# Kernel optimization log

Measured on AMD Instinct MI355X. Metric: run time of the kernel, lower is better.

Reference implementation:

```python
import jax, jax.numpy as jnp
import numpy as np

CODEBOOK_SIZE = 8192
LATENT_DIM = 256
COMMIT_W = 0.25
B, H, W = 32, 32, 32


def setup_inputs() -> dict:
    key = jax.random.key(0)
    kz, ke = jax.random.split(key)
    z = jax.random.normal(kz, (B, LATENT_DIM, H, W), dtype=jnp.float32)
    # torch init: uniform(-1/K, 1/K)
    emb = jax.random.uniform(ke, (CODEBOOK_SIZE, LATENT_DIM), dtype=jnp.float32,
                             minval=-1.0 / CODEBOOK_SIZE, maxval=1.0 / CODEBOOK_SIZE)
    return {"z": z, "emb": emb}


def reference(z, emb):
    # (B,C,H,W) -> (B,H,W,C)
    zp = jnp.transpose(z, (0, 2, 3, 1))
    zf = zp.reshape(-1, LATENT_DIM)                      # (N, D)
    # squared-distance via expansion: ||z||^2 + ||e||^2 - 2 z.e
    d = (jnp.sum(zf * zf, axis=1, keepdims=True)
         + jnp.sum(emb * emb, axis=1)[None, :]
         - 2.0 * jnp.matmul(zf, emb.T))                  # (N, K)
    idx = jnp.argmin(d, axis=1)                          # (N,)
    z_q = emb[idx].reshape(zp.shape)                     # (B,H,W,C)
    zq_sg = jax.lax.stop_gradient(z_q)
    z_sg = jax.lax.stop_gradient(zp)
    codebook_loss = (COMMIT_W * jnp.mean((zq_sg - zp) ** 2)
                     + jnp.mean((z_q - z_sg) ** 2))
    # straight-through estimator
    z_q_st = zp + jax.lax.stop_gradient(z_q - zp)
    quantized = jnp.transpose(z_q_st, (0, 3, 1, 2))      # (B,C,H,W)
    indices = idx.reshape(zp.shape[:-1])                 # (B,H,W)
    return quantized, indices, codebook_loss
```

## Files before the change

### kernel.cpp

```cpp
#include <hip/hip_runtime.h>

typedef _Float16 half_t;
typedef _Float16 half8 __attribute__((ext_vector_type(8)));
typedef _Float16 half2_t __attribute__((ext_vector_type(2)));
typedef float f32x4 __attribute__((ext_vector_type(4)));
typedef unsigned long long ull;

#define K_CODES 8192
#define D_DIM   256
#define N_PTS   32768
#define HW      1024
#define CHW     262144
#define B_      32
#define W_      32

#define OFF_IDX  8388608
#define OFF_LOSS 8421376

#define KSPLIT 4
#define KRANGE 2048
#define NCHUNK 32
#define W_WIN  1.5e-4f
#define WX_SEL 0.63f
#define CAP_BKT 2048

#define WS_E16  0x000000u
#define WS_E2   0x400000u
#define WS_Z2   0x408000u
#define WS_FLAG 0x428000u
#define WS_SEL8 0x450000u
#define WS_SCNT 0x490000u
#define WS_PART 0x4B0000u
#define WS_BCNT 0x4B2000u
#define DO_CMAX  0x000000u
#define DO_ENT   0x000000u
#define DO_PTOP  0x100000u
#define DO_CAND  0x500000u
#define DO_FSCAN 0x900000u
#define DO_CCNT  0x920000u
#define DO_Z16   0x1000000u

__device__ __forceinline__ unsigned int mono_enc(float f) {
    unsigned int u = __float_as_uint(f);
    return (u & 0x80000000u) ? ~u : (u | 0x80000000u);
}
__device__ __forceinline__ float mono_dec(unsigned int m) {
    unsigned int u = (m & 0x80000000u) ? (m ^ 0x80000000u) : ~m;
    return __uint_as_float(u);
}
__device__ __forceinline__ void glds16(const void* g, void* l) {
    __builtin_amdgcn_global_load_lds(
        (const __attribute__((address_space(1))) unsigned int*)g,
        (__attribute__((address_space(3))) unsigned int*)l, 16, 0, 0);
}

union u32h2 { unsigned int u; half2_t h; };
__device__ __forceinline__ half2_t h2(unsigned int u) { u32h2 t; t.u = u; return t.h; }

#if __has_builtin(__builtin_amdgcn_fdot2)
__device__ __forceinline__ float fdot2_(half2_t a, half2_t b, float c) {
    return __builtin_amdgcn_fdot2(a, b, c, false);
}
#else
__device__ __forceinline__ float fdot2_(half2_t a, half2_t b, float c) {
    return fmaf((float)a.x, (float)b.x, fmaf((float)a.y, (float)b.y, c));
}
#endif

__device__ __forceinline__ float red8np(const float* r) {
    return __fadd_rn(__fadd_rn(__fadd_rn(r[0], r[1]), __fadd_rn(r[2], r[3])),
                     __fadd_rn(__fadd_rn(r[4], r[5]), __fadd_rn(r[6], r[7])));
}

__global__ __launch_bounds__(256) void convert_kernel(
        const float* __restrict__ emb, char* __restrict__ e16, float* __restrict__ e2,
        const float* __restrict__ z, half_t* __restrict__ z16, float* __restrict__ z2,
        int* __restrict__ flags) {
    const int bx = blockIdx.x;
    if (bx < 32) {
        if (bx == 0 && threadIdx.x == 0) flags[0] = 0;
        const int k = bx * 256 + threadIdx.x;
        const float4* row = (const float4*)(emb + (size_t)k * D_DIM);
        char* dst = e16 + (size_t)(k >> 6) * 32768 + (size_t)(k & 63) * 16;
        float r[8], h1 = 0.f;
        #pragma unroll 4
        for (int s = 0; s < 32; s++) {
            if (s == 16) { h1 = red8np(r); }
            const float4 v0 = row[s * 2];
            const float4 v1 = row[s * 2 + 1];
            union { half_t h[8]; uint4 u; } t;
            t.h[0] = (half_t)(v0.x * 8192.0f); t.h[1] = (half_t)(v0.y * 8192.0f);
            t.h[2] = (half_t)(v0.z * 8192.0f); t.h[3] = (half_t)(v0.w * 8192.0f);
            t.h[4] = (half_t)(v1.x * 8192.0f); t.h[5] = (half_t)(v1.y * 8192.0f);
            t.h[6] = (half_t)(v1.z * 8192.0f); t.h[7] = (half_t)(v1.w * 8192.0f);
            *(uint4*)(dst + (size_t)s * 1024) = t.u;
            const float q0 = __fmul_rn(v0.x, v0.x), q1 = __fmul_rn(v0.y, v0.y);
            const float q2 = __fmul_rn(v0.z, v0.z), q3 = __fmul_rn(v0.w, v0.w);
            const float q4 = __fmul_rn(v1.x, v1.x), q5 = __fmul_rn(v1.y, v1.y);
            const float q6 = __fmul_rn(v1.z, v1.z), q7 = __fmul_rn(v1.w, v1.w);
            if (s == 0 || s == 16) {
                r[0] = q0; r[1] = q1; r[2] = q2; r[3] = q3;
                r[4] = q4; r[5] = q5; r[6] = q6; r[7] = q7;
            } else {
                r[0] = __fadd_rn(r[0], q0); r[1] = __fadd_rn(r[1], q1);
                r[2] = __fadd_rn(r[2], q2); r[3] = __fadd_rn(r[3], q3);
                r[4] = __fadd_rn(r[4], q4); r[5] = __fadd_rn(r[5], q5);
                r[6] = __fadd_rn(r[6], q6); r[7] = __fadd_rn(r[7], q7);
            }
        }
        e2[k] = __fadd_rn(h1, red8np(r));
    } else {
        const int pt = (bx - 32) * 256 + threadIdx.x;
        const float* zp = z + (size_t)(pt >> 10) * CHW + (pt & (HW - 1));
        half_t* dst = z16 + (size_t)pt * 256;
        float hs[2];
        #pragma unroll
        for (int hb = 0; hb < 2; hb++) {
            float r[8];
            #pragma unroll
            for (int d0 = 0; d0 < 128; d0 += 8) {
                union { half_t h[8]; uint4 u; } t;
                #pragma unroll
                for (int j = 0; j < 8; j++) {
                    const float v = zp[(size_t)(hb * 128 + d0 + j) * HW];
                    t.h[j] = (half_t)v;
                    const float sq = __fmul_rn(v, v);
                    r[j] = (d0 == 0) ? sq : __fadd_rn(r[j], sq);
                }
                *(uint4*)(dst + hb * 128 + d0) = t.u;
            }
            hs[hb] = red8np(r);
        }
        z2[pt] = __fadd_rn(hs[0], hs[1]);
    }
}

__global__ __launch_bounds__(512, 4) void pass1_kernel(
        const half_t* __restrict__ z16, const uint4* __restrict__ e16,
        float* __restrict__ cmax) {
    __shared__ __align__(16) char sA[65536];
    const int tid  = threadIdx.x;
    const int lane = tid & 63;
    const int wave = tid >> 6;
    const int col  = lane & 15;
    const int quad = lane >> 4;
    const int bx = blockIdx.x, by = blockIdx.y;
    const int p0 = bx * 256;
    const int kbase = by * KRANGE;

    half8 zb[2][8];
    #pragma unroll
    for (int n = 0; n < 2; n++) {
        const int pt = p0 + wave * 32 + n * 16 + col;
        const char* src = (const char*)z16 + (size_t)pt * 512 + quad * 16;
        #pragma unroll
        for (int ks = 0; ks < 8; ks++)
            zb[n][ks] = *(const half8*)(src + ks * 64);
    }

    const char* esrc = (const char*)e16 + (size_t)kbase * 512;
    {
        const char* s0 = esrc + wave * 4096 + lane * 16;
        char* d0 = sA + wave * 4096;
        #pragma unroll
        for (int i = 0; i < 4; i++) glds16(s0 + i * 1024, d0 + i * 1024);
    }
    __syncthreads();

    int cur = 0;
    for (int c = 0; c < NCHUNK; ++c) {
        if (c + 1 < NCHUNK) {
            const char* s0 = esrc + (size_t)(c + 1) * 32768 + wave * 4096 + lane * 16;
            char* d0 = sA + (cur ^ 1) * 32768 + wave * 4096;
            #pragma unroll
            for (int i = 0; i < 4; i++) glds16(s0 + i * 1024, d0 + i * 1024);
        }
        f32x4 acc[4][2];
        #pragma unroll
        for (int m = 0; m < 4; m++)
            #pragma unroll
            for (int n = 0; n < 2; n++) acc[m][n] = (f32x4){0.f, 0.f, 0.f, 0.f};

        const char* base = sA + cur * 32768 + col * 16;
        #pragma unroll
        for (int ks = 0; ks < 8; ks++) {
            const int so = (ks * 4 + quad) * 1024;
            half8 a[4];
            #pragma unroll
            for (int m = 0; m < 4; m++) a[m] = *(const half8*)(base + so + m * 256);
            #pragma unroll
            for (int m = 0; m < 4; m++)
                #pragma unroll
                for (int n = 0; n < 2; n++)
                    acc[m][n] = __builtin_amdgcn_mfma_f32_16x16x32_f16(a[m], zb[n][ks], acc[m][n], 0, 0, 0);
        }
        const int sub = by * NCHUNK + c;
        #pragma unroll
        for (int n = 0; n < 2; n++) {
            float xm = acc[0][n][0];
            #pragma unroll
            for (int m = 0; m < 4; m++)
                #pragma unroll
                for (int r = 0; r < 4; r++) xm = fmaxf(xm, acc[m][n][r]);
            xm = fmaxf(xm, __shfl_xor(xm, 16, 64));
            xm = fmaxf(xm, __shfl_xor(xm, 32, 64));
            if (quad == 0)
                cmax[(size_t)sub * N_PTS + p0 + wave * 32 + n * 16 + col] = xm;
        }
        __syncthreads();
        cur ^= 1;
    }
}

__global__ __launch_bounds__(256) void stageb_kernel(
        const float* __restrict__ cmax, ull* __restrict__ sel8, int* __restrict__ scnt,
        unsigned* __restrict__ bcnt) {
    if (threadIdx.x == 0) bcnt[blockIdx.x] = 0u;
    if (blockIdx.x == 0 && threadIdx.x == 1) bcnt[128] = 0u;
    const int pt = blockIdx.x * 256 + threadIdx.x;
    float xmax = -3.0e38f;
    #pragma unroll 8
    for (int s = 0; s < 128; s++) xmax = fmaxf(xmax, cmax[(size_t)s * N_PTS + pt]);
    const float cut = xmax - WX_SEL;
    ull pack = 0; int cnt = 0;
    for (int s = 0; s < 128; s++) {
        if (cmax[(size_t)s * N_PTS + pt] >= cut) {
            if (cnt < 8) pack |= ((ull)(unsigned)s) << (8 * cnt);
            cnt++;
        }
    }
    sel8[pt] = pack; scnt[pt] = cnt;
}

__global__ __launch_bounds__(256) void stageb2_kernel(
        const ull* __restrict__ sel8, int* __restrict__ scnt,
        unsigned* __restrict__ bcnt, unsigned* __restrict__ ent,
        unsigned* __restrict__ fslist, unsigned* __restrict__ ccnt) {
    const int pt = blockIdx.x * 256 + threadIdx.x;
    ccnt[pt] = 0u;
    const int cnt = scnt[pt];
    bool ok = (cnt >= 1 && cnt <= 8);
    if (ok) {
        const ull s8 = sel8[pt];
        for (int j = 0; j < cnt; j++) {
            const int s = (int)((s8 >> (8 * j)) & 0xFFu);
            const unsigned pos = atomicAdd(&bcnt[s], 1u);
            if (pos >= CAP_BKT) { ok = false; break; }
            ent[s * CAP_BKT + pos] = (unsigned)pt | ((unsigned)j << 16);
        }
    }
    if (!ok) {
        const unsigned mp = atomicAdd(&bcnt[128], 1u);
        fslist[mp] = (unsigned)pt;
        scnt[pt] = -1;
    }
}

__global__ __launch_bounds__(256) void stagec3_kernel(
        const half_t* __restrict__ z16, const uint4* __restrict__ e16,
        const unsigned* __restrict__ bcnt, const unsigned* __restrict__ ent,
        ull* __restrict__ ptop, unsigned* __restrict__ cand,
        unsigned* __restrict__ ccnt) {
    __shared__ __align__(16) unsigned int zslot[4][128];
    const int tid = threadIdx.x, lane = tid & 63, wave = tid >> 6;
    const int c = blockIdx.x & 127, part = blockIdx.x >> 7;
    const int npart = gridDim.x >> 7;
    const unsigned cnt = min(bcnt[c], (unsigned)CAP_BKT);
    if (cnt == 0) return;
    const int code = c * 64 + lane;
    uint4 e[32];
    {
        const uint4* er = e16 + (size_t)(code >> 6) * 2048 + (code & 63);
        #pragma unroll
        for (int j = 0; j < 32; j++) e[j] = er[(size_t)j * 64];
    }
    const char* zb = (const char*)&zslot[wave][0];
    for (unsigned i = (unsigned)(part * 4 + wave); i < cnt; i += (unsigned)(npart * 4)) {
        const unsigned ev = ent[c * CAP_BKT + i];
        const int pt = (int)(ev & 0xFFFFu);
        const int j  = (int)((ev >> 16) & 7u);
        {
            const uint2 w = *(const uint2*)((const char*)z16 + (size_t)pt * 512 + lane * 8);
            *(uint2*)((char*)&zslot[wave][0] + lane * 8) = w;
        }
        __threadfence_block();
        float x0 = 0.f, x1 = 0.f, x2 = 0.f, x3 = 0.f, x4 = 0.f, x5 = 0.f, x6 = 0.f, x7 = 0.f;
        #pragma unroll
        for (int q = 0; q < 32; q += 2) {
            const uint4 z0 = *(const uint4*)(zb + q * 16);
            const uint4 z1 = *(const uint4*)(zb + q * 16 + 16);
            x0 = fdot2_(h2(e[q].x),     h2(z0.x), x0);
            x1 = fdot2_(h2(e[q].y),     h2(z0.y), x1);
            x2 = fdot2_(h2(e[q].z),     h2(z0.z), x2);
            x3 = fdot2_(h2(e[q].w),     h2(z0.w), x3);
            x4 = fdot2_(h2(e[q + 1].x), h2(z1.x), x4);
            x5 = fdot2_(h2(e[q + 1].y), h2(z1.y), x5);
            x6 = fdot2_(h2(e[q + 1].z), h2(z1.z), x6);
            x7 = fdot2_(h2(e[q + 1].w), h2(z1.w), x7);
        }
        const float sc = (((x0 + x1) + (x2 + x3)) + ((x4 + x5) + (x6 + x7))) * (-2.0f / 8192.0f);
        ull r1 = ((ull)mono_enc(sc) << 32) | (unsigned)code;
        ull r2 = ~0ull;
        #pragma unroll
        for (int s = 1; s < 64; s <<= 1) {
            const ull o1 = __shfl_xor(r1, s, 64);
            const ull o2 = __shfl_xor(r2, s, 64);
            if (o1 < r1) { r2 = (r1 < o2) ? r1 : o2; r1 = o1; }
            else         { r2 = (o1 < r2) ? o1 : r2; }
        }
        if (lane == 0) {
            ptop[(size_t)(pt * 8 + j) * 2 + 0] = r1;
            ptop[(size_t)(pt * 8 + j) * 2 + 1] = r2;
        }
        const float v1 = mono_dec((unsigned)(r1 >> 32));
        const bool in = sc < v1 + W_WIN;
        const ull m = __ballot(in);
        int base = 0;
        if (lane == 0) base = (int)atomicAdd(&ccnt[pt], (unsigned)__popcll(m));
        base = __shfl(base, 0, 64);
        const int p = base + (int)__popcll(m & ((1ull << lane) - 1ull));
        if (in && p < 32) cand[(size_t)pt * 32 + p] = (unsigned)code;
    }
}

__global__ __launch_bounds__(256) void mergec_kernel(
        const ull* __restrict__ ptop, const int* __restrict__ scnt,
        int* __restrict__ flags, float* __restrict__ dout) {
    const int pt = blockIdx.x * 256 + threadIdx.x;
    const int cnt = scnt[pt];
    if (cnt < 1 || cnt > 8) return;
    ull b1 = ~0ull, b2 = ~0ull;
    for (int j = 0; j < cnt; j++) {
        #pragma unroll
        for (int t = 0; t < 2; t++) {
            const ull v = ptop[(size_t)(pt * 8 + j) * 2 + t];
            if (v < b1) { b2 = b1; b1 = v; } else if (v < b2) b2 = v;
        }
    }
    dout[OFF_IDX + pt] = (float)(unsigned)(b1 & 0xFFFFFFFFu);
    const float v1 = mono_dec((unsigned)(b1 >> 32));
    const float v2 = mono_dec((unsigned)(b2 >> 32));
    if (v2 - v1 < W_WIN) {
        const int pos = atomicAdd(flags, 1);
        flags[16 + pos] = pt;
    }
}

__global__ __launch_bounds__(256) void refine_kernel(
        const float* __restrict__ z, const float* __restrict__ emb,
        const float* __restrict__ e2, const float* __restrict__ z2,
        const unsigned* __restrict__ cand, const unsigned* __restrict__ candcnt,
        const int* __restrict__ flags, const unsigned* __restrict__ fslist,
        const unsigned* __restrict__ bcnt, float* __restrict__ dout) {
    __shared__ float zl[4][256];
    const int tid = threadIdx.x, lane = tid & 63, wave = tid >> 6;
    const int gw = blockIdx.x * 4 + wave;
    const int nw = gridDim.x * 4;
    const int count = flags[0];
    for (int f = gw; f < count; f += nw) {
        const int n = flags[16 + f];
        const float* zp = z + (size_t)(n >> 10) * CHW + (n & (HW - 1));
        #pragma unroll
        for (int q = 0; q < 4; q++)
            zl[wave][lane + 64 * q] = zp[(size_t)(lane + 64 * q) * HW];
        __threadfence_block();
        int cc = (int)candcnt[n]; if (cc > 32) cc = 32;
        float d; int k;
        if (lane < cc) {
            k = (int)cand[(size_t)n * 32 + lane];
            const float* ep = emb + (size_t)k * D_DIM;
            float m = 0.f;
            for (int c = 0; c < D_DIM; c++) m = fmaf(zl[wave][c], ep[c], m);
            d = __fsub_rn(__fadd_rn(z2[n], e2[k]), __fmul_rn(2.0f, m));
        } else { d = 3.0e38f; k = 1 << 20; }
        #pragma unroll
        for (int s = 1; s < 32; s <<= 1) {
            const float od = __shfl_xor(d, s, 64);
            const int   ok = __shfl_xor(k, s, 64);
            if (od < d || (od == d && ok < k)) { d = od; k = ok; }
        }
        if (lane == 0) dout[OFF_IDX + n] = (float)k;
    }
    const int fscount = (int)bcnt[128];
    for (int f = gw; f < fscount; f += nw) {
        const int n = (int)fslist[f];
        const float* zp = z + (size_t)(n >> 10) * CHW + (n & (HW - 1));
        #pragma unroll
        for (int q = 0; q < 4; q++)
            zl[wave][lane + 64 * q] = zp[(size_t)(lane + 64 * q) * HW];
        __threadfence_block();
        float bd = 3.0e38f; int bk = 1 << 20;
        for (int t = 0; t < K_CODES / 64; t++) {
            const int k = t * 64 + lane;
            const float* ep = emb + (size_t)k * D_DIM;
            float m = 0.f;
            for (int c = 0; c < D_DIM; c++) m = fmaf(zl[wave][c], ep[c], m);
            const float d = __fsub_rn(__fadd_rn(z2[n], e2[k]), __fmul_rn(2.0f, m));
            if (d < bd) { bd = d; bk = k; }
        }
        #pragma unroll
        for (int s = 1; s < 64; s <<= 1) {
            const float od = __shfl_xor(bd, s, 64);
            const int   ok = __shfl_xor(bk, s, 64);
            if (od < bd || (od == bd && ok < bk)) { bd = od; bk = ok; }
        }
        if (lane == 0) dout[OFF_IDX + n] = (float)bk;
    }
}

__global__ __launch_bounds__(256) void gather_kernel(
        const float* __restrict__ z, const float* __restrict__ emb,
        float* __restrict__ dout, float* __restrict__ partials) {
    __shared__ __align__(16) float qs[D_DIM][W_ + 1];
    __shared__ float red[4];
    const int bh = blockIdx.x;
    const int b = bh >> 5, h = bh & 31;
    const int tid = threadIdx.x;

    const float* idxf = dout + OFF_IDX + bh * W_;
    const int w  = tid >> 3;
    const int cq = tid & 7;
    const int idx_w = (int)idxf[w];
    const float* erow = emb + (size_t)idx_w * D_DIM;
    #pragma unroll
    for (int it = 0; it < 8; it++) {
        const int c4 = (it * 8 + cq) * 4;
        float4 v = *(const float4*)(erow + c4);
        qs[c4 + 0][w] = v.x; qs[c4 + 1][w] = v.y;
        qs[c4 + 2][w] = v.z; qs[c4 + 3][w] = v.w;
    }
    __syncthreads();

    const int w2 = tid & 31, cg = tid >> 5;
    float ss = 0.f;
    const float* zbh = z    + (size_t)b * CHW + h * W_;
    float*       obh = dout + (size_t)b * CHW + h * W_;
    #pragma unroll
    for (int it = 0; it < 32; it++) {
        const int c = cg * 32 + it;
        const float q  = qs[c][w2];
        const float zv = zbh[(size_t)c * HW + w2];
        obh[(size_t)c * HW + w2] = q;
        const float dd = q - zv;
        ss = fmaf(dd, dd, ss);
    }
    #pragma unroll
    for (int m = 1; m < 64; m <<= 1) ss += __shfl_xor(ss, m, 64);
    const int lane = tid & 63, wv = tid >> 6;
    if (lane == 0) red[wv] = ss;
    __syncthreads();
    if (tid == 0) partials[bh] = red[0] + red[1] + red[2] + red[3];
}

__global__ void loss_kernel(const float* __restrict__ partials, float* __restrict__ dout) {
    __shared__ float sv[256];
    const int tid = threadIdx.x;
    float s = 0.f;
    #pragma unroll
    for (int i = 0; i < 4; i++) s += partials[tid + 256 * i];
    sv[tid] = s;
    __syncthreads();
    for (int st = 128; st > 0; st >>= 1) {
        if (tid < st) sv[tid] += sv[tid + st];
        __syncthreads();
    }
    if (tid == 0) dout[OFF_LOSS] = sv[0] * (1.25f / 8388608.0f);
}

extern "C" void kernel_launch(void* const* d_in, const int* in_sizes, int n_in,
                              void* d_out, int out_size, void* d_ws, size_t ws_size,
                              hipStream_t stream) {
    const float* z   = (const float*)d_in[0];
    const float* emb = (const float*)d_in[1];
    float* dout = (float*)d_out;

    char* ws  = (char*)d_ws;
    char* dob = (char*)d_out;
    uint4*  e16   = (uint4*)(ws + WS_E16);
    float*  e2    = (float*)(ws + WS_E2);
    float*  z2    = (float*)(ws + WS_Z2);
    int*    flags = (int*)(ws + WS_FLAG);
    ull*    sel8  = (ull*)(ws + WS_SEL8);
    int*    scnt  = (int*)(ws + WS_SCNT);
    float*  part  = (float*)(ws + WS_PART);
    unsigned* bcnt = (unsigned*)(ws + WS_BCNT);
    float*    cmax  = (float*)(dob + DO_CMAX);
    half_t*   z16   = (half_t*)(dob + DO_Z16);
    unsigned* ent   = (unsigned*)(dob + DO_ENT);
    ull*      ptop  = (ull*)(dob + DO_PTOP);
    unsigned* cand  = (unsigned*)(dob + DO_CAND);
    unsigned* fslist= (unsigned*)(dob + DO_FSCAN);
    unsigned* ccnt  = (unsigned*)(dob + DO_CCNT);

    hipLaunchKernelGGL(convert_kernel, dim3(160),         dim3(256), 0, stream, emb, (char*)e16, e2, z, z16, z2, flags);
    hipLaunchKernelGGL(pass1_kernel,   dim3(128, KSPLIT), dim3(512), 0, stream, z16, e16, cmax);
    hipLaunchKernelGGL(stageb_kernel,  dim3(128),         dim3(256), 0, stream, cmax, sel8, scnt, bcnt);
    hipLaunchKernelGGL(stageb2_kernel, dim3(128),         dim3(256), 0, stream, sel8, scnt, bcnt, ent, fslist, ccnt);
    hipLaunchKernelGGL(stagec3_kernel, dim3(1024),        dim3(256), 0, stream, z16, e16, bcnt, ent, ptop, cand, ccnt);
    hipLaunchKernelGGL(mergec_kernel,  dim3(128),         dim3(256), 0, stream, ptop, scnt, flags, dout);
    hipLaunchKernelGGL(refine_kernel,  dim3(512),         dim3(256), 0, stream, z, emb, e2, z2, cand, ccnt, flags, fslist, bcnt, dout);
    hipLaunchKernelGGL(gather_kernel,  dim3(B_ * 32),     dim3(256), 0, stream, z, emb, dout, part);
    hipLaunchKernelGGL(loss_kernel,    dim3(1),           dim3(256), 0, stream, part, dout);
}
```

Baseline: 312.2 us.

## Fuse merge and refine kernels, atomic row max, and atomic loss reduction

Pass1 now keeps a per-point running max and publishes it with atomicMax into the index output area, so stageb no longer rescans all 128 cmax slices to find the max. The merge and refine kernels are combined into one wave-per-point kernel that either writes the winner directly, refines over the candidate list, or falls back to a full scan. The loss is accumulated with atomicAdd in gather, which removes the separate loss kernel. Two launches are dropped, but the fused kernel walks all 32768 points one wave at a time, which may load-balance worse than the flagged-list approach, and the float atomic loss sum is non-deterministic.

```diff
diff --git a/kernel.cpp b/kernel.cpp
--- a/kernel.cpp
+++ b/kernel.cpp
@@ -27,10 +27,8 @@
 #define WS_E16  0x000000u
 #define WS_E2   0x400000u
 #define WS_Z2   0x408000u
-#define WS_FLAG 0x428000u
 #define WS_SEL8 0x450000u
 #define WS_SCNT 0x490000u
-#define WS_PART 0x4B0000u
 #define WS_BCNT 0x4B2000u
 #define DO_CMAX  0x000000u
 #define DO_ENT   0x000000u
@@ -75,10 +73,10 @@
 __global__ __launch_bounds__(256) void convert_kernel(
         const float* __restrict__ emb, char* __restrict__ e16, float* __restrict__ e2,
         const float* __restrict__ z, half_t* __restrict__ z16, float* __restrict__ z2,
-        int* __restrict__ flags) {
+        float* __restrict__ dout) {
     const int bx = blockIdx.x;
     if (bx < 32) {
-        if (bx == 0 && threadIdx.x == 0) flags[0] = 0;
+        if (bx == 0 && threadIdx.x == 0) dout[OFF_LOSS] = 0.0f;
         const int k = bx * 256 + threadIdx.x;
         const float4* row = (const float4*)(emb + (size_t)k * D_DIM);
         char* dst = e16 + (size_t)(k >> 6) * 32768 + (size_t)(k & 63) * 16;
@@ -111,6 +109,7 @@
         e2[k] = __fadd_rn(h1, red8np(r));
     } else {
         const int pt = (bx - 32) * 256 + threadIdx.x;
+        ((unsigned*)(dout + OFF_IDX))[pt] = 0u;
         const float* zp = z + (size_t)(pt >> 10) * CHW + (pt & (HW - 1));
         half_t* dst = z16 + (size_t)pt * 256;
         float hs[2];
@@ -137,7 +136,7 @@
 
 __global__ __launch_bounds__(512, 4) void pass1_kernel(
         const half_t* __restrict__ z16, const uint4* __restrict__ e16,
-        float* __restrict__ cmax) {
+        float* __restrict__ cmax, unsigned* __restrict__ xatom) {
     __shared__ __align__(16) char sA[65536];
     const int tid  = threadIdx.x;
     const int lane = tid & 63;
@@ -167,6 +166,7 @@
     }
     __syncthreads();
 
+    float rmax[2] = {-3.0e38f, -3.0e38f};
     int cur = 0;
     for (int c = 0; c < NCHUNK; ++c) {
         if (c + 1 < NCHUNK) {
@@ -204,24 +204,27 @@
                 for (int r = 0; r < 4; r++) xm = fmaxf(xm, acc[m][n][r]);
             xm = fmaxf(xm, __shfl_xor(xm, 16, 64));
             xm = fmaxf(xm, __shfl_xor(xm, 32, 64));
+            rmax[n] = fmaxf(rmax[n], xm);
             if (quad == 0)
                 cmax[(size_t)sub * N_PTS + p0 + wave * 32 + n * 16 + col] = xm;
         }
         __syncthreads();
         cur ^= 1;
     }
+    if (quad == 0) {
+        #pragma unroll
+        for (int n = 0; n < 2; n++)
+            atomicMax(&xatom[p0 + wave * 32 + n * 16 + col], mono_enc(rmax[n]));
+    }
 }
 
 __global__ __launch_bounds__(256) void stageb_kernel(
-        const float* __restrict__ cmax, ull* __restrict__ sel8, int* __restrict__ scnt,
-        unsigned* __restrict__ bcnt) {
+        const float* __restrict__ cmax, const unsigned* __restrict__ xatom,
+        ull* __restrict__ sel8, int* __restrict__ scnt, unsigned* __restrict__ bcnt) {
     if (threadIdx.x == 0) bcnt[blockIdx.x] = 0u;
     if (blockIdx.x == 0 && threadIdx.x == 1) bcnt[128] = 0u;
     const int pt = blockIdx.x * 256 + threadIdx.x;
-    float xmax = -3.0e38f;
-    #pragma unroll 8
-    for (int s = 0; s < 128; s++) xmax = fmaxf(xmax, cmax[(size_t)s * N_PTS + pt]);
-    const float cut = xmax - WX_SEL;
+    const float cut = mono_dec(xatom[pt]) - WX_SEL;
     ull pack = 0; int cnt = 0;
     for (int s = 0; s < 128; s++) {
         if (cmax[(size_t)s * N_PTS + pt] >= cut) {
@@ -323,94 +326,83 @@
     }
 }
 
-__global__ __launch_bounds__(256) void mergec_kernel(
-        const ull* __restrict__ ptop, const int* __restrict__ scnt,
-        int* __restrict__ flags, float* __restrict__ dout) {
-    const int pt = blockIdx.x * 256 + threadIdx.x;
-    const int cnt = scnt[pt];
-    if (cnt < 1 || cnt > 8) return;
-    ull b1 = ~0ull, b2 = ~0ull;
-    for (int j = 0; j < cnt; j++) {
-        #pragma unroll
-        for (int t = 0; t < 2; t++) {
-            const ull v = ptop[(size_t)(pt * 8 + j) * 2 + t];
-            if (v < b1) { b2 = b1; b1 = v; } else if (v < b2) b2 = v;
-        }
-    }
-    dout[OFF_IDX + pt] = (float)(unsigned)(b1 & 0xFFFFFFFFu);
-    const float v1 = mono_dec((unsigned)(b1 >> 32));
-    const float v2 = mono_dec((unsigned)(b2 >> 32));
-    if (v2 - v1 < W_WIN) {
-        const int pos = atomicAdd(flags, 1);
-        flags[16 + pos] = pt;
-    }
-}
-
-__global__ __launch_bounds__(256) void refine_kernel(
+__global__ __launch_bounds__(256) void mergeref_kernel(
         const float* __restrict__ z, const float* __restrict__ emb,
         const float* __restrict__ e2, const float* __restrict__ z2,
-        const unsigned* __restrict__ cand, const unsigned* __restrict__ candcnt,
-        const int* __restrict__ flags, const unsigned* __restrict__ fslist,
-        const unsigned* __restrict__ bcnt, float* __restrict__ dout) {
+        const ull* __restrict__ ptop, const int* __restrict__ scnt,
+        const unsigned* __restrict__ cand, const unsigned* __restrict__ ccnt,
+        float* __restrict__ dout) {
     __shared__ float zl[4][256];
     const int tid = threadIdx.x, lane = tid & 63, wave = tid >> 6;
     const int gw = blockIdx.x * 4 + wave;
     const int nw = gridDim.x * 4;
-    const int count = flags[0];
-    for (int f = gw; f < count; f += nw) {
-        const int n = flags[16 + f];
-        const float* zp = z + (size_t)(n >> 10) * CHW + (n & (HW - 1));
-        #pragma unroll
-        for (int q = 0; q < 4; q++)
-            zl[wave][lane + 64 * q] = zp[(size_t)(lane + 64 * q) * HW];
-        __threadfence_block();
-        int cc = (int)candcnt[n]; if (cc > 32) cc = 32;
-        float d; int k;
-        if (lane < cc) {
-            k = (int)cand[(size_t)n * 32 + lane];
-            const float* ep = emb + (size_t)k * D_DIM;
-            float m = 0.f;
-            for (int c = 0; c < D_DIM; c++) m = fmaf(zl[wave][c], ep[c], m);
-            d = __fsub_rn(__fadd_rn(z2[n], e2[k]), __fmul_rn(2.0f, m));
-        } else { d = 3.0e38f; k = 1 << 20; }
-        #pragma unroll
-        for (int s = 1; s < 32; s <<= 1) {
-            const float od = __shfl_xor(d, s, 64);
-            const int   ok = __shfl_xor(k, s, 64);
-            if (od < d || (od == d && ok < k)) { d = od; k = ok; }
-        }
-        if (lane == 0) dout[OFF_IDX + n] = (float)k;
-    }
-    const int fscount = (int)bcnt[128];
-    for (int f = gw; f < fscount; f += nw) {
-        const int n = (int)fslist[f];
-        const float* zp = z + (size_t)(n >> 10) * CHW + (n & (HW - 1));
-        #pragma unroll
-        for (int q = 0; q < 4; q++)
-            zl[wave][lane + 64 * q] = zp[(size_t)(lane + 64 * q) * HW];
-        __threadfence_block();
-        float bd = 3.0e38f; int bk = 1 << 20;
-        for (int t = 0; t < K_CODES / 64; t++) {
-            const int k = t * 64 + lane;
-            const float* ep = emb + (size_t)k * D_DIM;
-            float m = 0.f;
-            for (int c = 0; c < D_DIM; c++) m = fmaf(zl[wave][c], ep[c], m);
-            const float d = __fsub_rn(__fadd_rn(z2[n], e2[k]), __fmul_rn(2.0f, m));
-            if (d < bd) { bd = d; bk = k; }
-        }
-        #pragma unroll
-        for (int s = 1; s < 64; s <<= 1) {
-            const float od = __shfl_xor(bd, s, 64);
-            const int   ok = __shfl_xor(bk, s, 64);
-            if (od < bd || (od == bd && ok < bk)) { bd = od; bk = ok; }
-        }
-        if (lane == 0) dout[OFF_IDX + n] = (float)bk;
+    for (int pt = gw; pt < N_PTS; pt += nw) {
+        const int cnt = scnt[pt];
+        if (cnt >= 1 && cnt <= 8) {
+            ull b1 = ~0ull, b2 = ~0ull;
+            for (int j = 0; j < cnt; j++) {
+                #pragma unroll
+                for (int t = 0; t < 2; t++) {
+                    const ull v = ptop[(size_t)(pt * 8 + j) * 2 + t];
+                    if (v < b1) { b2 = b1; b1 = v; } else if (v < b2) b2 = v;
+                }
+            }
+            const float v1 = mono_dec((unsigned)(b1 >> 32));
+            const float v2 = mono_dec((unsigned)(b2 >> 32));
+            if (v2 - v1 >= W_WIN) {
+                if (lane == 0) dout[OFF_IDX + pt] = (float)(unsigned)(b1 & 0xFFFFFFFFu);
+                continue;
+            }
+            const float* zp = z + (size_t)(pt >> 10) * CHW + (pt & (HW - 1));
+            #pragma unroll
+            for (int q = 0; q < 4; q++)
+                zl[wave][lane + 64 * q] = zp[(size_t)(lane + 64 * q) * HW];
+            __threadfence_block();
+            int cc = (int)ccnt[pt]; if (cc > 32) cc = 32;
+            float d; int k;
+            if (lane < cc) {
+                k = (int)cand[(size_t)pt * 32 + lane];
+                const float* ep = emb + (size_t)k * D_DIM;
+                float m = 0.f;
+                for (int c = 0; c < D_DIM; c++) m = fmaf(zl[wave][c], ep[c], m);
+                d = __fsub_rn(__fadd_rn(z2[pt], e2[k]), __fmul_rn(2.0f, m));
+            } else { d = 3.0e38f; k = 1 << 20; }
+            #pragma unroll
+            for (int s = 1; s < 32; s <<= 1) {
+                const float od = __shfl_xor(d, s, 64);
+                const int   ok = __shfl_xor(k, s, 64);
+                if (od < d || (od == d && ok < k)) { d = od; k = ok; }
+            }
+            if (lane == 0) dout[OFF_IDX + pt] = (float)k;
+        } else {
+            const float* zp = z + (size_t)(pt >> 10) * CHW + (pt & (HW - 1));
+            #pragma unroll
+            for (int q = 0; q < 4; q++)
+                zl[wave][lane + 64 * q] = zp[(size_t)(lane + 64 * q) * HW];
+            __threadfence_block();
+            float bd = 3.0e38f; int bk = 1 << 20;
+            for (int t = 0; t < K_CODES / 64; t++) {
+                const int k = t * 64 + lane;
+                const float* ep = emb + (size_t)k * D_DIM;
+                float m = 0.f;
+                for (int c = 0; c < D_DIM; c++) m = fmaf(zl[wave][c], ep[c], m);
+                const float d = __fsub_rn(__fadd_rn(z2[pt], e2[k]), __fmul_rn(2.0f, m));
+                if (d < bd) { bd = d; bk = k; }
+            }
+            #pragma unroll
+            for (int s = 1; s < 64; s <<= 1) {
+                const float od = __shfl_xor(bd, s, 64);
+                const int   ok = __shfl_xor(bk, s, 64);
+                if (od < bd || (od == bd && ok < bk)) { bd = od; bk = ok; }
+            }
+            if (lane == 0) dout[OFF_IDX + pt] = (float)bk;
+        }
     }
 }
 
 __global__ __launch_bounds__(256) void gather_kernel(
         const float* __restrict__ z, const float* __restrict__ emb,
-        float* __restrict__ dout, float* __restrict__ partials) {
+        float* __restrict__ dout) {
     __shared__ __align__(16) float qs[D_DIM][W_ + 1];
     __shared__ float red[4];
     const int bh = blockIdx.x;
@@ -449,22 +441,10 @@
     const int lane = tid & 63, wv = tid >> 6;
     if (lane == 0) red[wv] = ss;
     __syncthreads();
-    if (tid == 0) partials[bh] = red[0] + red[1] + red[2] + red[3];
-}
-
-__global__ void loss_kernel(const float* __restrict__ partials, float* __restrict__ dout) {
-    __shared__ float sv[256];
-    const int tid = threadIdx.x;
-    float s = 0.f;
-    #pragma unroll
-    for (int i = 0; i < 4; i++) s += partials[tid + 256 * i];
-    sv[tid] = s;
-    __syncthreads();
-    for (int st = 128; st > 0; st >>= 1) {
-        if (tid < st) sv[tid] += sv[tid + st];
-        __syncthreads();
-    }
-    if (tid == 0) dout[OFF_LOSS] = sv[0] * (1.25f / 8388608.0f);
+    if (tid == 0) {
+        const float t = red[0] + red[1] + red[2] + red[3];
+        atomicAdd(dout + OFF_LOSS, t * (1.25f / 8388608.0f));
+    }
 }
 
 extern "C" void kernel_launch(void* const* d_in, const int* in_sizes, int n_in,
@@ -479,10 +459,8 @@
     uint4*  e16   = (uint4*)(ws + WS_E16);
     float*  e2    = (float*)(ws + WS_E2);
     float*  z2    = (float*)(ws + WS_Z2);
-    int*    flags = (int*)(ws + WS_FLAG);
     ull*    sel8  = (ull*)(ws + WS_SEL8);
     int*    scnt  = (int*)(ws + WS_SCNT);
-    float*  part  = (float*)(ws + WS_PART);
     unsigned* bcnt = (unsigned*)(ws + WS_BCNT);
     float*    cmax  = (float*)(dob + DO_CMAX);
     half_t*   z16   = (half_t*)(dob + DO_Z16);
@@ -491,14 +469,13 @@
     unsigned* cand  = (unsigned*)(dob + DO_CAND);
     unsigned* fslist= (unsigned*)(dob + DO_FSCAN);
     unsigned* ccnt  = (unsigned*)(dob + DO_CCNT);
-
-    hipLaunchKernelGGL(convert_kernel, dim3(160),         dim3(256), 0, stream, emb, (char*)e16, e2, z, z16, z2, flags);
-    hipLaunchKernelGGL(pass1_kernel,   dim3(128, KSPLIT), dim3(512), 0, stream, z16, e16, cmax);
-    hipLaunchKernelGGL(stageb_kernel,  dim3(128),         dim3(256), 0, stream, cmax, sel8, scnt, bcnt);
+    unsigned* xatom = (unsigned*)(dout + OFF_IDX);
+
+    hipLaunchKernelGGL(convert_kernel, dim3(160),         dim3(256), 0, stream, emb, (char*)e16, e2, z, z16, z2, dout);
+    hipLaunchKernelGGL(pass1_kernel,   dim3(128, KSPLIT), dim3(512), 0, stream, z16, e16, cmax, xatom);
+    hipLaunchKernelGGL(stageb_kernel,  dim3(128),         dim3(256), 0, stream, cmax, xatom, sel8, scnt, bcnt);
     hipLaunchKernelGGL(stageb2_kernel, dim3(128),         dim3(256), 0, stream, sel8, scnt, bcnt, ent, fslist, ccnt);
     hipLaunchKernelGGL(stagec3_kernel, dim3(1024),        dim3(256), 0, stream, z16, e16, bcnt, ent, ptop, cand, ccnt);
-    hipLaunchKernelGGL(mergec_kernel,  dim3(128),         dim3(256), 0, stream, ptop, scnt, flags, dout);
-    hipLaunchKernelGGL(refine_kernel,  dim3(512),         dim3(256), 0, stream, z, emb, e2, z2, cand, ccnt, flags, fslist, bcnt, dout);
-    hipLaunchKernelGGL(gather_kernel,  dim3(B_ * 32),     dim3(256), 0, stream, z, emb, dout, part);
-    hipLaunchKernelGGL(loss_kernel,    dim3(1),           dim3(256), 0, stream, part, dout);
-}
+    hipLaunchKernelGGL(mergeref_kernel,dim3(256),         dim3(256), 0, stream, z, emb, e2, z2, ptop, scnt, cand, ccnt, dout);
+    hipLaunchKernelGGL(gather_kernel,  dim3(B_ * 32),     dim3(256), 0, stream, z, emb, dout);
+}
```

New measurement: 364.3 us. 16.7% more time.
